# Performance work log

Hardware: AMD Instinct MI355X
Metric: run time of the kernel (lower is better)

The kernel has to match this reference:

```python
import jax, jax.numpy as jnp
import numpy as np

EMBED_DIM = 1024


def setup_inputs() -> dict:
    key = jax.random.key(0)
    ks = jax.random.split(key, 7)
    B, S, D = 4, 2048, EMBED_DIM
    scale = 1.0 / np.sqrt(D)
    x = jax.random.normal(ks[0], (B, S, D), dtype=jnp.float32)
    # nn.Linear weights stored as [out, in]; we keep [in, out] for x @ W
    Wq = jax.random.normal(ks[1], (D, D), dtype=jnp.float32) * scale
    bq = jax.random.normal(ks[2], (D,), dtype=jnp.float32) * scale
    Wk = jax.random.normal(ks[3], (D, D), dtype=jnp.float32) * scale
    bk = jax.random.normal(ks[4], (D,), dtype=jnp.float32) * scale
    Wv = jax.random.normal(ks[5], (D, D), dtype=jnp.float32) * scale
    bv = jax.random.normal(ks[6], (D,), dtype=jnp.float32) * scale
    return {"x": x, "Wq": Wq, "bq": bq, "Wk": Wk, "bk": bk, "Wv": Wv, "bv": bv}


def reference(x, Wq, bq, Wk, bk, Wv, bv):
    # Single-head attention (num_heads unused in original module).
    q = x @ Wq + bq            # [B, S, D]
    k = x @ Wk + bk            # [B, S, D]
    v = x @ Wv + bv            # [B, S, D]
    inv_sqrt_d = 1.0 / jnp.sqrt(jnp.asarray(x.shape[-1], x.dtype))
    scores = jnp.einsum("bsd,btd->bst", q, k) * inv_sqrt_d  # [B, S, S]
    attn = jax.nn.softmax(scores, axis=-1)
    return jnp.einsum("bst,btd->bsd", attn, v)
```

## Files before the change

kernel.cpp:

```cpp
#include <hip/hip_runtime.h>
#include <hip/hip_bf16.h>


using floatx4 = __attribute__((ext_vector_type(4))) float;
using shortx8 = __attribute__((ext_vector_type(8))) short;
using shortx4 = __attribute__((ext_vector_type(4))) short;

__device__ __forceinline__ short f2bf(float f) {
    __hip_bfloat16 h = __float2bfloat16(f);
    return *reinterpret_cast<short*>(&h);
}
__device__ __forceinline__ float bf2f(short s) {
    unsigned u = (unsigned)(unsigned short)s << 16;
    return __uint_as_float(u);
}

#define MFMA16(a, b, c) __builtin_amdgcn_mfma_f32_16x16x32_bf16((a), (b), (c), 0, 0, 0)

__device__ __forceinline__ void gld_lds16(const void* g, void* l) {
    __builtin_amdgcn_global_load_lds(
        (const __attribute__((address_space(1))) void*)g,
        (__attribute__((address_space(3))) void*)l, 16, 0, 0);
}

template<int MH>
__device__ __forceinline__ void rdA(const short* sAb, int wm, int lrow,
                                    int xo0, int xo1, shortx8 (&af)[4][2]) {
    const short* base = sAb + ((wm << 7) + (MH << 6) + lrow) * 64;
#pragma unroll
    for (int i = 0; i < 4; ++i) {
        af[i][0] = *reinterpret_cast<const shortx8*>(base + i * 1024 + xo0);
        af[i][1] = *reinterpret_cast<const shortx8*>(base + i * 1024 + xo1);
    }
}
template<int NH>
__device__ __forceinline__ void rdB(const short* sBb, int wn, int lrow,
                                    int xo0, int xo1, shortx8 (&bf)[4][2]) {
    const short* base = sBb + ((wn << 6) + (NH << 5) + lrow) * 64;
#pragma unroll
    for (int j = 0; j < 2; ++j) {
        bf[NH * 2 + j][0] = *reinterpret_cast<const shortx8*>(base + j * 1024 + xo0);
        bf[NH * 2 + j][1] = *reinterpret_cast<const shortx8*>(base + j * 1024 + xo1);
    }
}
template<int MH, int NH>
__device__ __forceinline__ void mfq(shortx8 (&af)[4][2], shortx8 (&bf)[4][2],
                                    floatx4 (&acc)[8][4]) {
    __builtin_amdgcn_s_setprio(1);
#pragma unroll
    for (int i = 0; i < 4; ++i) {
#pragma unroll
        for (int j = 0; j < 2; ++j) {
            acc[MH * 4 + i][NH * 2 + j] =
                MFMA16(af[i][0], bf[NH * 2 + j][0], acc[MH * 4 + i][NH * 2 + j]);
            acc[MH * 4 + i][NH * 2 + j] =
                MFMA16(af[i][1], bf[NH * 2 + j][1], acc[MH * 4 + i][NH * 2 + j]);
        }
    }
    __builtin_amdgcn_s_setprio(0);
}

__device__ __forceinline__ void gemm256_loop8(
    const short* __restrict__ A, const short* __restrict__ B,
    int lda, int ldb, int K,
    short* sA, short* sB, floatx4 (&acc)[8][4], int t)
{
    const int w = t >> 6, l = t & 63;
    const int wm = w >> 2, wn = w & 3;
    const int lrow = l & 15, quad = l >> 4, r8 = lrow & 7;
    const int xo0 = (quad ^ r8) << 3;
    const int xo1 = ((quad + 4) ^ r8) << 3;
    const int rr = t >> 3;
    const int gsw = ((t & 7) ^ (rr & 7)) << 3;
    const short* gA0 = A + (size_t)rr * lda + gsw;
    const short* gA1 = A + (size_t)(128 + rr) * lda + gsw;
    const short* gB0 = B + (size_t)rr * ldb + gsw;
    const short* gB1 = B + (size_t)(128 + rr) * ldb + gsw;
    const int wofs = w << 9;

    auto stage = [&](const short* g, int ld, int kt, short* ldsb) {
        const short* p = g + kt;
        gld_lds16(p, ldsb + wofs);
        gld_lds16(p + (size_t)(ld << 6), ldsb + wofs + 4096);
    };

    shortx8 af[4][2], bf[4][2];
    const int NT = K >> 6;

    stage(gA0, lda, 0, sA);
    stage(gA1, lda, 0, sA + 8192);
    stage(gB0, ldb, 0, sB);
    stage(gB1, ldb, 0, sB + 8192);
    stage(gB0, ldb, 64, sB + 16384);
    stage(gB1, ldb, 64, sB + 16384 + 8192);
    asm volatile("s_waitcnt vmcnt(4)" ::: "memory");
    __builtin_amdgcn_s_barrier();

    for (int T = 0; T < NT; T += 2) {
        const bool more = (T + 2) < NT;
        const int ktA1 = (T + 1) << 6;
        const int ktN2 = (T + 2) << 6;
        const int ktB3 = (T + 3) << 6;
        short* sA0 = sA;           short* sB0 = sB;
        short* sA1 = sA + 16384;   short* sB1 = sB + 16384;

        rdA<0>(sA0, wm, lrow, xo0, xo1, af);
        rdB<0>(sB0, wn, lrow, xo0, xo1, bf);
        stage(gA0, lda, ktA1, sA1);
        asm volatile("s_waitcnt lgkmcnt(8)" ::: "memory");
        __builtin_amdgcn_s_barrier();
        asm volatile("s_waitcnt lgkmcnt(0)" ::: "memory");
        __builtin_amdgcn_sched_barrier(0);
        mfq<0, 0>(af, bf, acc);
        __builtin_amdgcn_s_barrier();

        rdB<1>(sB0, wn, lrow, xo0, xo1, bf);
        stage(gA1, lda, ktA1, sA1 + 8192);
        __builtin_amdgcn_s_barrier();
        asm volatile("s_waitcnt lgkmcnt(0)" ::: "memory");
        __builtin_amdgcn_sched_barrier(0);
        mfq<0, 1>(af, bf, acc);
        __builtin_amdgcn_s_barrier();

        rdA<1>(sA0, wm, lrow, xo0, xo1, af);
        if (more) stage(gB0, ldb, ktN2, sB0);
        __builtin_amdgcn_s_barrier();
        asm volatile("s_waitcnt lgkmcnt(0)" ::: "memory");
        __builtin_amdgcn_sched_barrier(0);
        mfq<1, 0>(af, bf, acc);
        __builtin_amdgcn_s_barrier();

        if (more) stage(gB1, ldb, ktN2, sB0 + 8192);
        __builtin_amdgcn_s_barrier();
        __builtin_amdgcn_sched_barrier(0);
        mfq<1, 1>(af, bf, acc);
        if (more) { asm volatile("s_waitcnt vmcnt(4)" ::: "memory"); }
        else      { asm volatile("s_waitcnt vmcnt(0)" ::: "memory"); }
        __builtin_amdgcn_s_barrier();

        rdA<0>(sA1, wm, lrow, xo0, xo1, af);
        rdB<0>(sB1, wn, lrow, xo0, xo1, bf);
        if (more) stage(gA0, lda, ktN2, sA0);
        asm volatile("s_waitcnt lgkmcnt(8)" ::: "memory");
        __builtin_amdgcn_s_barrier();
        asm volatile("s_waitcnt lgkmcnt(0)" ::: "memory");
        __builtin_amdgcn_sched_barrier(0);
        mfq<0, 0>(af, bf, acc);
        __builtin_amdgcn_s_barrier();

        rdB<1>(sB1, wn, lrow, xo0, xo1, bf);
        if (more) stage(gA1, lda, ktN2, sA0 + 8192);
        __builtin_amdgcn_s_barrier();
        asm volatile("s_waitcnt lgkmcnt(0)" ::: "memory");
        __builtin_amdgcn_sched_barrier(0);
        mfq<0, 1>(af, bf, acc);
        __builtin_amdgcn_s_barrier();

        rdA<1>(sA1, wm, lrow, xo0, xo1, af);
        if (more) stage(gB0, ldb, ktB3, sB1);
        __builtin_amdgcn_s_barrier();
        asm volatile("s_waitcnt lgkmcnt(0)" ::: "memory");
        __builtin_amdgcn_sched_barrier(0);
        mfq<1, 0>(af, bf, acc);
        __builtin_amdgcn_s_barrier();

        if (more) stage(gB1, ldb, ktB3, sB1 + 8192);
        __builtin_amdgcn_s_barrier();
        __builtin_amdgcn_sched_barrier(0);
        mfq<1, 1>(af, bf, acc);
        if (more) { asm volatile("s_waitcnt vmcnt(4)" ::: "memory"); }
        __builtin_amdgcn_s_barrier();
    }
}

__device__ __forceinline__ void gemm_loop(
    const short* __restrict__ A, const short* __restrict__ B,
    size_t lda, size_t ldb, int K,
    short* as_, short* bs_, floatx4 (&acc)[4][4], int w, int l)
{
    const int lr8 = l >> 3;
    const int swz = ((l & 7) ^ lr8) * 8;
    const int lrow = l & 15, quad = l >> 4;
    const int wr = w >> 1, wc = w & 1;
    const int r8r = lrow & 7;
    const short* pa = A + (size_t)(w * 32 + lr8) * lda + swz;
    const short* pb = B + (size_t)(w * 32 + lr8) * ldb + swz;
    short* la = as_ + w * 4 * 512;
    short* lb = bs_ + w * 4 * 512;

    for (int kt = 0; kt < K; kt += 64) {
        for (int c = 0; c < 4; ++c) {
            gld_lds16(pa + (size_t)c * 8 * lda + kt, la + c * 512);
            gld_lds16(pb + (size_t)c * 8 * ldb + kt, lb + c * 512);
        }
        __syncthreads();
        for (int kk = 0; kk < 64; kk += 32) {
            const int xoff = (((kk >> 3) + quad) ^ r8r) << 3;
            shortx8 af[4], bfr[4];
            for (int i = 0; i < 4; ++i)
                af[i] = *reinterpret_cast<const shortx8*>(
                    &as_[(size_t)(wr * 64 + i * 16 + lrow) * 64 + xoff]);
            for (int j = 0; j < 4; ++j)
                bfr[j] = *reinterpret_cast<const shortx8*>(
                    &bs_[(size_t)(wc * 64 + j * 16 + lrow) * 64 + xoff]);
            for (int i = 0; i < 4; ++i)
                for (int j = 0; j < 4; ++j)
                    acc[i][j] = MFMA16(af[i], bfr[j], acc[i][j]);
        }
        __syncthreads();
    }
}

__global__ __launch_bounds__(256) void prep_kernel(
    const float* __restrict__ X,
    const float* __restrict__ Wq, const float* __restrict__ Wk,
    const float* __restrict__ Wv,
    const float* __restrict__ bq, const float* __restrict__ bk,
    const float* __restrict__ bv,
    short* __restrict__ Xb, short* __restrict__ Wt,
    float* __restrict__ bcat)
{
    const int id = blockIdx.x, t = threadIdx.x;
    if (id < 4096) {
        size_t i = ((size_t)id * 256 + t) * 8;
        float4 v0 = *reinterpret_cast<const float4*>(X + i);
        float4 v1 = *reinterpret_cast<const float4*>(X + i + 4);
        shortx8 s;
        s[0] = f2bf(v0.x); s[1] = f2bf(v0.y); s[2] = f2bf(v0.z); s[3] = f2bf(v0.w);
        s[4] = f2bf(v1.x); s[5] = f2bf(v1.y); s[6] = f2bf(v1.z); s[7] = f2bf(v1.w);
        *reinterpret_cast<shortx8*>(Xb + i) = s;
    } else if (id < 4864) {
        __shared__ float tl[64][65];
        const int wid = id - 4096;
        const int z = wid >> 8, t16 = wid & 255;
        const float* src = (z == 0) ? Wq : (z == 1) ? Wk : Wv;
        short* dst = Wt + (size_t)z * 1024 * 1024;
        const int k0 = (t16 >> 4) * 64, n0 = (t16 & 15) * 64;
        for (int i = t; i < 64 * 64; i += 256) {
            int r = i >> 6, c = i & 63;
            tl[r][c] = src[(size_t)(k0 + r) * 1024 + n0 + c];
        }
        __syncthreads();
        for (int i = t; i < 64 * 64; i += 256) {
            int r = i >> 6, c = i & 63;
            dst[(size_t)(n0 + r) * 1024 + k0 + c] = f2bf(tl[c][r]);
        }
    } else {
        const int z = id - 4864;
        const float* bsrc = (z == 0) ? bq : (z == 1) ? bk : bv;
        for (int i = t; i < 1024; i += 256) bcat[z * 1024 + i] = bsrc[i];
    }
}

__global__ __launch_bounds__(256) void qkv_v_kernel(
    const short* __restrict__ Xb, const short* __restrict__ Wt,
    const float* __restrict__ bcat, short* __restrict__ Vt)
{
    __shared__ short as_[128 * 64];
    __shared__ short bs_[128 * 64];
    const int t = threadIdx.x, w = t >> 6, l = t & 63;
    const int m0 = blockIdx.x * 128;
    const int n0 = 2048 + blockIdx.y * 128;
    const int wr = w >> 1, wc = w & 1, lrow = l & 15, quad = l >> 4;

    floatx4 acc[4][4];
    for (int i = 0; i < 4; ++i)
        for (int j = 0; j < 4; ++j) acc[i][j] = floatx4{0.f, 0.f, 0.f, 0.f};

    gemm_loop(Xb + (size_t)m0 * 1024, Wt + (size_t)n0 * 1024,
              1024, 1024, 1024, as_, bs_, acc, w, l);

    for (int i = 0; i < 4; ++i) {
        int rbase = m0 + wr * 64 + i * 16 + quad * 4;
        int b = rbase >> 11, sl = rbase & 2047;
        for (int j = 0; j < 4; ++j) {
            int coln = n0 + wc * 64 + j * 16 + lrow;
            int col = coln & 1023;
            float bvv = bcat[coln];
            shortx4 s;
            for (int r = 0; r < 4; ++r) s[r] = f2bf(acc[i][j][r] + bvv);
            *reinterpret_cast<shortx4*>(
                &Vt[((size_t)b * 1024 + col) * 2048 + sl]) = s;
        }
    }
}

__global__ __launch_bounds__(512, 2) void qkv_qk_kernel(
    const short* __restrict__ Xb, const short* __restrict__ Wt,
    const float* __restrict__ bcat, short* __restrict__ dQ,
    short* __restrict__ dK)
{
    __shared__ short sA[2 * 16384];
    __shared__ short sB[2 * 16384];
    const int t = threadIdx.x;
    const int m0 = blockIdx.x * 256, n0 = blockIdx.y * 256;
    const int w = t >> 6, l = t & 63;
    const int wm = w >> 2, wn = w & 3, lrow = l & 15, quad = l >> 4;
    const int sec = n0 >> 10;

    floatx4 acc[8][4];
#pragma unroll
    for (int i = 0; i < 8; ++i)
#pragma unroll
        for (int j = 0; j < 4; ++j) acc[i][j] = floatx4{0.f, 0.f, 0.f, 0.f};

    gemm256_loop8(Xb + (size_t)m0 * 1024, Wt + (size_t)n0 * 1024,
                  1024, 1024, 1024, sA, sB, acc, t);

    short* outN = (sec == 0) ? dQ : dK;
#pragma unroll
    for (int i = 0; i < 8; ++i) {
        int rbase = m0 + wm * 128 + i * 16 + quad * 4;
#pragma unroll
        for (int j = 0; j < 4; ++j) {
            int coln = n0 + wn * 64 + j * 16 + lrow;
            int col = coln & 1023;
            float bvv = bcat[coln];
#pragma unroll
            for (int r = 0; r < 4; ++r)
                outN[(size_t)(rbase + r) * 1024 + col] =
                    f2bf(acc[i][j][r] + bvv);
        }
    }
}

__global__ __launch_bounds__(512, 2) void scores_kernel(
    const short* __restrict__ dQ, const short* __restrict__ dK,
    short* __restrict__ P, float* __restrict__ partials, int row_start)
{
    __shared__ short sA[2 * 16384];
    __shared__ short sB[2 * 16384];
    const int t = threadIdx.x;
    int bx = blockIdx.x, by = blockIdx.y;
    if (gridDim.x == 32) {
        const int c = bx & 7;
        const int k = (bx >> 3) + (by << 2);
        const int bb = c >> 1, half = c & 1;
        bx = bb * 8 + (k & 3) + 4 * half;
        by = k >> 2;
    }
    const int m0 = bx * 256;
    const int n0 = by * 256;
    const int g0 = row_start + m0;
    const int b = g0 >> 11;
    const int w = t >> 6, l = t & 63;
    const int wm = w >> 2, wn = w & 3, lrow = l & 15, quad = l >> 4;

    floatx4 acc[8][4];
#pragma unroll
    for (int i = 0; i < 8; ++i)
#pragma unroll
        for (int j = 0; j < 4; ++j) acc[i][j] = floatx4{0.f, 0.f, 0.f, 0.f};

    gemm256_loop8(dQ + (size_t)g0 * 1024, dK + ((size_t)b * 2048 + n0) * 1024,
                  1024, 1024, 1024, sA, sB, acc, t);

    float* sred = reinterpret_cast<float*>(sA);
#pragma unroll
    for (int i = 0; i < 8; ++i) {
        int rl = wm * 128 + i * 16 + quad * 4;
        int rloc = m0 + rl;
        float rs[4] = {0.f, 0.f, 0.f, 0.f};
#pragma unroll
        for (int j = 0; j < 4; ++j) {
            int col = n0 + wn * 64 + j * 16 + lrow;
#pragma unroll
            for (int r = 0; r < 4; ++r) {
                short pb = f2bf(__expf(acc[i][j][r] * 0.03125f - 20.0f));
                P[(size_t)(rloc + r) * 2048 + col] = pb;
                rs[r] += bf2f(pb);
            }
        }
#pragma unroll
        for (int r = 0; r < 4; ++r)
            for (int m = 1; m <= 8; m <<= 1)
                rs[r] += __shfl_xor(rs[r], m, 64);
        if (lrow == 0)
#pragma unroll
            for (int r = 0; r < 4; ++r)
                sred[(rl + r) * 4 + wn] = rs[r];
    }
    __syncthreads();
    if (t < 256) {
        float s = sred[t * 4] + sred[t * 4 + 1] + sred[t * 4 + 2] + sred[t * 4 + 3];
        partials[(size_t)(row_start + m0 + t) * 8 + by] = s;
    }
}

__global__ __launch_bounds__(256) void pv_kernel(
    const short* __restrict__ P, const short* __restrict__ Vt,
    const float* __restrict__ partials, float* __restrict__ Out, int row_start)
{
    __shared__ short as_[128 * 64];
    __shared__ short bs_[128 * 64];
    const int t = threadIdx.x, w = t >> 6, l = t & 63;
    int bx = blockIdx.x, by = blockIdx.y;
    if (gridDim.x == 64) {
        const int c = bx & 7;
        const int k = (bx >> 3) + (by << 3);
        const int bb = c >> 1, half = c & 1;
        bx = bb * 16 + (k & 7) + 8 * half;
        by = k >> 3;
    }
    const int m0 = bx * 128;
    const int n0 = by * 128;
    const int g0 = row_start + m0;
    const int b = g0 >> 11;
    const int wr = w >> 1, wc = w & 1, lrow = l & 15, quad = l >> 4;

    floatx4 acc[4][4];
    for (int i = 0; i < 4; ++i)
        for (int j = 0; j < 4; ++j) acc[i][j] = floatx4{0.f, 0.f, 0.f, 0.f};

    gemm_loop(P + (size_t)m0 * 2048, Vt + ((size_t)b * 1024 + n0) * 2048,
              2048, 2048, 2048, as_, bs_, acc, w, l);

    for (int i = 0; i < 4; ++i) {
        int rloc = m0 + wr * 64 + i * 16 + quad * 4;
        int rglb = row_start + rloc;
        float is[4];
        for (int r = 0; r < 4; ++r) {
            const float4* pp =
                reinterpret_cast<const float4*>(&partials[(size_t)(rglb + r) * 8]);
            float4 p0 = pp[0], p1 = pp[1];
            float s = (p0.x + p0.y) + (p0.z + p0.w) +
                      (p1.x + p1.y) + (p1.z + p1.w);
            is[r] = 1.0f / s;
        }
        for (int j = 0; j < 4; ++j) {
            int col = n0 + wc * 64 + j * 16 + lrow;
            for (int r = 0; r < 4; ++r)
                Out[(size_t)(rglb + r) * 1024 + col] = acc[i][j][r] * is[r];
        }
    }
}

extern "C" void kernel_launch(void* const* d_in, const int* in_sizes, int n_in,
                              void* d_out, int out_size, void* d_ws, size_t ws_size,
                              hipStream_t stream)
{
    const float* x  = (const float*)d_in[0];
    const float* Wq = (const float*)d_in[1];
    const float* bq = (const float*)d_in[2];
    const float* Wk = (const float*)d_in[3];
    const float* bk = (const float*)d_in[4];
    const float* Wv = (const float*)d_in[5];
    const float* bv = (const float*)d_in[6];
    float* out = (float*)d_out;

    short* dQ = (short*)d_out;
    short* dK = dQ + (size_t)8192 * 1024;

    char* ws = (char*)d_ws;
    short* Wt   = (short*)ws;
    float* bcat = (float*)(ws + 6291456);
    float* partials = (float*)(ws + 6291456 + 12288);
    short* Vt   = (short*)(ws + 6291456 + 12288 + 262144);
    char*  region = ws + 6291456 + 12288 + 262144 + 16777216;
    const size_t base = 6291456 + 12288 + 262144 + 16777216;

    size_t avail = ws_size > base ? ws_size - base : 0;
    long rows_fit = (long)(avail / 4096);
    int chunk = (int)(rows_fit & ~255L);
    if (chunk > 8192) chunk = 8192;
    if (chunk < 256) chunk = 256;
    short* Xb = (short*)region;
    short* P  = (short*)region;

    prep_kernel<<<dim3(4867), 256, 0, stream>>>(x, Wq, Wk, Wv, bq, bk, bv,
                                                Xb, Wt, bcat);
    qkv_v_kernel<<<dim3(64, 8), 256, 0, stream>>>(Xb, Wt, bcat, Vt);
    qkv_qk_kernel<<<dim3(32, 8), 512, 0, stream>>>(Xb, Wt, bcat, dQ, dK);

    for (int rs = 0; rs < 8192; rs += chunk) {
        int rows = 8192 - rs;
        if (rows > chunk) rows = chunk;
        scores_kernel<<<dim3(rows / 256, 8), 512, 0, stream>>>(dQ, dK, P, partials, rs);
        pv_kernel<<<dim3(rows / 128, 8), 256, 0, stream>>>(P, Vt, partials, out, rs);
    }
}
```

Baseline: 232.7 us.

## Restructure 256x256 GEMM main loop into four phases with fewer barriers

Rewrites the double-buffered LDS pipeline of the 256-tile GEMM loop so each half-K step has two phases instead of four. Both B fragment halves are read at once and two MFMA quadrants are issued back to back. Global loads for the next tile are grouped (A0, B0, B1 together) and the vmcnt waits are retuned to match. This roughly halves the number of workgroup barriers per iteration and gives the loads longer to hide behind compute. The cost is higher register pressure and a riskier, hand-tuned wait-count schedule where an error would race on LDS.

```diff
diff --git a/kernel.cpp b/kernel.cpp
--- a/kernel.cpp
+++ b/kernel.cpp
@@ -60,7 +60,7 @@
     __builtin_amdgcn_s_setprio(0);
 }
 
-__device__ __forceinline__ void gemm256_loop8(
+__device__ __forceinline__ void gemm256_loop4(
     const short* __restrict__ A, const short* __restrict__ B,
     int lda, int ldb, int K,
     short* sA, short* sB, floatx4 (&acc)[8][4], int t)
@@ -86,89 +86,73 @@
 
     shortx8 af[4][2], bf[4][2];
     const int NT = K >> 6;
-
-    stage(gA0, lda, 0, sA);
-    stage(gA1, lda, 0, sA + 8192);
-    stage(gB0, ldb, 0, sB);
-    stage(gB1, ldb, 0, sB + 8192);
-    stage(gB0, ldb, 64, sB + 16384);
-    stage(gB1, ldb, 64, sB + 16384 + 8192);
-    asm volatile("s_waitcnt vmcnt(4)" ::: "memory");
+    short* sA0 = sA;           short* sB0 = sB;
+    short* sA1 = sA + 16384;   short* sB1 = sB + 16384;
+
+    stage(gA0, lda, 0, sA0); stage(gA1, lda, 0, sA0 + 8192);
+    stage(gB0, ldb, 0, sB0); stage(gB1, ldb, 0, sB0 + 8192);
+    stage(gA0, lda, 64, sA1);
+    stage(gB0, ldb, 64, sB1); stage(gB1, ldb, 64, sB1 + 8192);
+    asm volatile("s_waitcnt vmcnt(6)" ::: "memory");
     __builtin_amdgcn_s_barrier();
 
     for (int T = 0; T < NT; T += 2) {
         const bool more = (T + 2) < NT;
         const int ktA1 = (T + 1) << 6;
-        const int ktN2 = (T + 2) << 6;
-        const int ktB3 = (T + 3) << 6;
-        short* sA0 = sA;           short* sB0 = sB;
-        short* sA1 = sA + 16384;   short* sB1 = sB + 16384;
+        const int kt2  = (T + 2) << 6;
+        const int kt3  = (T + 3) << 6;
 
         rdA<0>(sA0, wm, lrow, xo0, xo1, af);
         rdB<0>(sB0, wn, lrow, xo0, xo1, bf);
-        stage(gA0, lda, ktA1, sA1);
+        rdB<1>(sB0, wn, lrow, xo0, xo1, bf);
+        stage(gA1, lda, ktA1, sA1 + 8192);
         asm volatile("s_waitcnt lgkmcnt(8)" ::: "memory");
         __builtin_amdgcn_s_barrier();
         asm volatile("s_waitcnt lgkmcnt(0)" ::: "memory");
         __builtin_amdgcn_sched_barrier(0);
         mfq<0, 0>(af, bf, acc);
-        __builtin_amdgcn_s_barrier();
-
-        rdB<1>(sB0, wn, lrow, xo0, xo1, bf);
-        stage(gA1, lda, ktA1, sA1 + 8192);
-        __builtin_amdgcn_s_barrier();
-        asm volatile("s_waitcnt lgkmcnt(0)" ::: "memory");
-        __builtin_amdgcn_sched_barrier(0);
         mfq<0, 1>(af, bf, acc);
         __builtin_amdgcn_s_barrier();
 
         rdA<1>(sA0, wm, lrow, xo0, xo1, af);
-        if (more) stage(gB0, ldb, ktN2, sB0);
+        if (more) {
+            stage(gA0, lda, kt2, sA0);
+            stage(gB0, ldb, kt2, sB0); stage(gB1, ldb, kt2, sB0 + 8192);
+        }
         __builtin_amdgcn_s_barrier();
         asm volatile("s_waitcnt lgkmcnt(0)" ::: "memory");
         __builtin_amdgcn_sched_barrier(0);
         mfq<1, 0>(af, bf, acc);
-        __builtin_amdgcn_s_barrier();
-
-        if (more) stage(gB1, ldb, ktN2, sB0 + 8192);
-        __builtin_amdgcn_s_barrier();
-        __builtin_amdgcn_sched_barrier(0);
         mfq<1, 1>(af, bf, acc);
-        if (more) { asm volatile("s_waitcnt vmcnt(4)" ::: "memory"); }
-        else      { asm volatile("s_waitcnt vmcnt(0)" ::: "memory"); }
+        if (more) { asm volatile("s_waitcnt vmcnt(8)" ::: "memory"); }
+        else      { asm volatile("s_waitcnt vmcnt(2)" ::: "memory"); }
         __builtin_amdgcn_s_barrier();
 
         rdA<0>(sA1, wm, lrow, xo0, xo1, af);
         rdB<0>(sB1, wn, lrow, xo0, xo1, bf);
-        if (more) stage(gA0, lda, ktN2, sA0);
+        rdB<1>(sB1, wn, lrow, xo0, xo1, bf);
+        if (more) stage(gA1, lda, kt2, sA0 + 8192);
         asm volatile("s_waitcnt lgkmcnt(8)" ::: "memory");
         __builtin_amdgcn_s_barrier();
         asm volatile("s_waitcnt lgkmcnt(0)" ::: "memory");
         __builtin_amdgcn_sched_barrier(0);
         mfq<0, 0>(af, bf, acc);
-        __builtin_amdgcn_s_barrier();
-
-        rdB<1>(sB1, wn, lrow, xo0, xo1, bf);
-        if (more) stage(gA1, lda, ktN2, sA0 + 8192);
-        __builtin_amdgcn_s_barrier();
-        asm volatile("s_waitcnt lgkmcnt(0)" ::: "memory");
-        __builtin_amdgcn_sched_barrier(0);
         mfq<0, 1>(af, bf, acc);
+        if (more) { asm volatile("s_waitcnt vmcnt(8)" ::: "memory"); }
+        else      { asm volatile("s_waitcnt vmcnt(0)" ::: "memory"); }
         __builtin_amdgcn_s_barrier();
 
         rdA<1>(sA1, wm, lrow, xo0, xo1, af);
-        if (more) stage(gB0, ldb, ktB3, sB1);
+        if (more) {
+            stage(gA0, lda, kt3, sA1);
+            stage(gB0, ldb, kt3, sB1); stage(gB1, ldb, kt3, sB1 + 8192);
+        }
         __builtin_amdgcn_s_barrier();
         asm volatile("s_waitcnt lgkmcnt(0)" ::: "memory");
         __builtin_amdgcn_sched_barrier(0);
         mfq<1, 0>(af, bf, acc);
-        __builtin_amdgcn_s_barrier();
-
-        if (more) stage(gB1, ldb, ktB3, sB1 + 8192);
-        __builtin_amdgcn_s_barrier();
-        __builtin_amdgcn_sched_barrier(0);
         mfq<1, 1>(af, bf, acc);
-        if (more) { asm volatile("s_waitcnt vmcnt(4)" ::: "memory"); }
+        if (more) { asm volatile("s_waitcnt vmcnt(6)" ::: "memory"); }
         __builtin_amdgcn_s_barrier();
     }
 }
@@ -304,7 +288,7 @@
 #pragma unroll
         for (int j = 0; j < 4; ++j) acc[i][j] = floatx4{0.f, 0.f, 0.f, 0.f};
 
-    gemm256_loop8(Xb + (size_t)m0 * 1024, Wt + (size_t)n0 * 1024,
+    gemm256_loop4(Xb + (size_t)m0 * 1024, Wt + (size_t)n0 * 1024,
                   1024, 1024, 1024, sA, sB, acc, t);
 
     short* outN = (sec == 0) ? dQ : dK;
@@ -352,7 +336,7 @@
 #pragma unroll
         for (int j = 0; j < 4; ++j) acc[i][j] = floatx4{0.f, 0.f, 0.f, 0.f};
 
-    gemm256_loop8(dQ + (size_t)g0 * 1024, dK + ((size_t)b * 2048 + n0) * 1024,
+    gemm256_loop4(dQ + (size_t)g0 * 1024, dK + ((size_t)b * 2048 + n0) * 1024,
                   1024, 1024, 1024, sA, sB, acc, t);
 
     float* sred = reinterpret_cast<float*>(sA);
```

Result: no change. 229.3 us (-1.5%).
